# Performance work log

Measured on AMD Instinct MI355X. Metric: run time of the kernel, lower is better.

The kernel has to match this reference:

```python
import jax, jax.numpy as jnp
import numpy as np

N = 50000      # nodes
E = 800000     # edges (last N are self-loops)
F_IN = 128     # n_feats
D = 64         # embedding_size (per-head out dim)
H = 3          # num_heads
G = 1024       # graphs in batch


def setup_inputs() -> dict:
    key = jax.random.key(0)
    ks = jax.random.split(key, 16)
    feats = jax.random.normal(ks[0], (N, F_IN), dtype=jnp.float32)
    # edges: random part + self-loops so every node has in-degree >= 1
    rs = jax.random.randint(ks[1], (E - N,), 0, N)
    rd = jax.random.randint(ks[2], (E - N,), 0, N)
    loops = jnp.arange(N)
    src = jnp.concatenate([rs, loops]).astype(jnp.int32)
    dst = jnp.concatenate([rd, loops]).astype(jnp.int32)
    graph_ids = jnp.sort(jax.random.randint(ks[3], (N,), 0, G)).astype(jnp.int32)

    def nrm(k, shape, fan_in):
        return jax.random.normal(k, shape, dtype=jnp.float32) * (1.0 / np.sqrt(fan_in))

    # gat1A params (DGL GATConv: fc no-bias, attn_l/attn_r [H,D], bias [H*D])
    W1 = nrm(ks[4], (F_IN, H * D), F_IN)
    al1 = nrm(ks[5], (H, D), D)
    ar1 = nrm(ks[6], (H, D), D)
    b1 = jnp.zeros((H * D,), jnp.float32)
    # gatn params (shared across the 2 loop iterations)
    W2 = nrm(ks[7], (D, H * D), D)
    al2 = nrm(ks[8], (H, D), D)
    ar2 = nrm(ks[9], (H, D), D)
    b2 = jnp.zeros((H * D,), jnp.float32)
    # linear1A (shared)
    Wl = nrm(ks[10], (H * D, D), H * D)
    bl = jnp.zeros((D,), jnp.float32)
    return {"feats": feats, "src": src, "dst": dst, "graph_ids": graph_ids,
            "W1": W1, "al1": al1, "ar1": ar1, "b1": b1,
            "W2": W2, "al2": al2, "ar2": ar2, "b2": b2,
            "Wl": Wl, "bl": bl}


def gat_conv(h, W, al, ar, b, src, dst):
    # h: [N, Fin] -> z: [N, H, D]
    z = (h @ W).reshape(-1, H, D)
    el = jnp.sum(z * al, axis=-1)   # [N, H]
    er = jnp.sum(z * ar, axis=-1)   # [N, H]
    e = jax.nn.leaky_relu(el[src] + er[dst], negative_slope=0.2)  # [E, H]
    # edge softmax over incoming edges of each dst node
    m = jax.ops.segment_max(e, dst, num_segments=N)
    ex = jnp.exp(e - m[dst])
    denom = jax.ops.segment_sum(ex, dst, num_segments=N)
    alpha = ex / denom[dst]                              # [E, H]
    msg = z[src] * alpha[:, :, None]                     # [E, H, D]
    out = jax.ops.segment_sum(msg, dst, num_segments=N)  # [N, H, D]
    return out + b.reshape(H, D)


def reference(feats, src, dst, graph_ids, W1, al1, ar1, b1, W2, al2, ar2, b2, Wl, bl):
    x = gat_conv(feats, W1, al1, ar1, b1, src, dst)   # [N, H, D]
    x = x.reshape(N, H * D)
    x = x @ Wl + bl                                   # [N, D]
    for _ in range(2):
        x = gat_conv(x, W2, al2, ar2, b2, src, dst)
        x = x.reshape(N, H * D)
        x = x @ Wl + bl
        # nn.LeakyReLU(True) -> negative_slope = 1.0 -> identity (faithful)
    # AvgPooling: per-graph mean of node features
    sums = jax.ops.segment_sum(x, graph_ids, num_segments=G)           # [G, D]
    cnts = jax.ops.segment_sum(jnp.ones((N,), x.dtype), graph_ids, num_segments=G)
    return sums / jnp.maximum(cnts, 1.0)[:, None]
```

## Files before the change

### kernel.cpp

```cpp
#include <hip/hip_runtime.h>
#include <hip/hip_bf16.h>

#define NN 50000
#define NE 800000
#define FIN 128
#define NHEADS 3
#define NG 1024
#define HD 192

typedef unsigned short ushort_t;
typedef __bf16 bf16x8 __attribute__((ext_vector_type(8)));
typedef float f32x4 __attribute__((ext_vector_type(4)));

__device__ __forceinline__ float bf2f(ushort_t u) {
    union { unsigned int i; float f; } c;
    c.i = ((unsigned int)u) << 16;
    return c.f;
}
__device__ __forceinline__ ushort_t f2bf(float f) {
    __hip_bfloat16 h = __float2bfloat16(f);
    return *reinterpret_cast<ushort_t*>(&h);
}

__global__ __launch_bounds__(256) void fconv_kernel(const float* __restrict__ f,
                                                    ushort_t* __restrict__ fb, int n4) {
    int i = blockIdx.x * 256 + threadIdx.x;
    if (i < n4) {
        float4 v = ((const float4*)f)[i];
        ushort4 o;
        o.x = f2bf(v.x); o.y = f2bf(v.y); o.z = f2bf(v.z); o.w = f2bf(v.w);
        ((ushort4*)fb)[i] = o;
    }
}

__global__ __launch_bounds__(256) void wconv_kernel(const float* __restrict__ W,
                                                    ushort_t* __restrict__ Wt, int K, int N) {
    int idx = blockIdx.x * 256 + threadIdx.x;
    if (idx < K * N) {
        int k = idx / N, n = idx - k * N;
        Wt[n * K + k] = f2bf(W[idx]);
    }
}

template<int K, int NT, int ATTN>
__global__ __launch_bounds__(256) void mgemm_kernel(const ushort_t* __restrict__ Ab,
                                                    const ushort_t* __restrict__ Wt,
                                                    const float* __restrict__ bias,
                                                    const float* __restrict__ al,
                                                    const float* __restrict__ ar,
                                                    float* __restrict__ el4,
                                                    float* __restrict__ er4,
                                                    float* __restrict__ xf,
                                                    ushort_t* __restrict__ xb,
                                                    ushort_t* __restrict__ zb,
                                                    int nrows) {
    constexpr int N = NT * 16;
    const int lane = threadIdx.x & 63;
    const int wid = threadIdx.x >> 6;
    const int row0 = blockIdx.x * 64 + wid * 16;
    const int m = lane & 15;
    const int kg = lane >> 4;

    int rA = row0 + m;
    if (rA > nrows - 1) rA = nrows - 1;
    const ushort_t* arow = Ab + (size_t)rA * K + kg * 8;

    const f32x4 zero4 = {0.f, 0.f, 0.f, 0.f};
    f32x4 acc[NT];
#pragma unroll
    for (int n = 0; n < NT; ++n) acc[n] = zero4;

#pragma unroll
    for (int k0 = 0; k0 < K; k0 += 32) {
        bf16x8 a = *(const bf16x8*)(arow + k0);
#pragma unroll
        for (int n = 0; n < NT; ++n) {
            bf16x8 b = *(const bf16x8*)(Wt + (size_t)(n * 16 + m) * K + k0 + kg * 8);
            acc[n] = __builtin_amdgcn_mfma_f32_16x16x32_bf16(a, b, acc[n], 0, 0, 0);
        }
    }

    const int orow = row0 + kg * 4;

    if (ATTN) {
        float sl[NHEADS][4], sr[NHEADS][4];
#pragma unroll
        for (int h = 0; h < NHEADS; ++h)
#pragma unroll
            for (int r = 0; r < 4; ++r) { sl[h][r] = 0.f; sr[h][r] = 0.f; }
#pragma unroll
        for (int n = 0; n < NT; ++n) {
            float alv = al[n * 16 + m];
            float arv = ar[n * 16 + m];
            const int h = n >> 2;
#pragma unroll
            for (int r = 0; r < 4; ++r) {
                sl[h][r] = fmaf(acc[n][r], alv, sl[h][r]);
                sr[h][r] = fmaf(acc[n][r], arv, sr[h][r]);
            }
        }
#pragma unroll
        for (int off = 1; off < 16; off <<= 1) {
#pragma unroll
            for (int h = 0; h < NHEADS; ++h)
#pragma unroll
                for (int r = 0; r < 4; ++r) {
                    sl[h][r] += __shfl_xor(sl[h][r], off);
                    sr[h][r] += __shfl_xor(sr[h][r], off);
                }
        }
#pragma unroll
        for (int r = 0; r < 4; ++r) {
            int gr = orow + r;
            if (gr < nrows) {
#pragma unroll
                for (int n = 0; n < NT; ++n)
                    zb[(size_t)gr * N + n * 16 + m] = f2bf(acc[n][r]);
                if (m == 0) {
                    *(float4*)(el4 + (size_t)gr * 4) = make_float4(sl[0][r], sl[1][r], sl[2][r], 0.f);
                    *(float4*)(er4 + (size_t)gr * 4) = make_float4(sr[0][r], sr[1][r], sr[2][r], 0.f);
                }
            }
        }
    } else {
#pragma unroll
        for (int r = 0; r < 4; ++r) {
            int gr = orow + r;
            if (gr < nrows) {
#pragma unroll
                for (int n = 0; n < NT; ++n) {
                    float v = acc[n][r] + bias[n * 16 + m];
                    xf[(size_t)gr * N + n * 16 + m] = v;
                    xb[(size_t)gr * N + n * 16 + m] = f2bf(v);
                }
            }
        }
    }
}

__global__ __launch_bounds__(256) void count_kernel(const int* __restrict__ dst,
                                                    int* __restrict__ cnt,
                                                    int* __restrict__ rank) {
    int e0 = blockIdx.x * 1024 + threadIdx.x;
#pragma unroll
    for (int k = 0; k < 4; ++k) {
        int e = e0 + k * 256;
        if (e < NE) rank[e] = atomicAdd(&cnt[dst[e]], 1);
    }
}

__global__ __launch_bounds__(256) void scan_block_kernel(const int* __restrict__ cnt,
                                                         int* __restrict__ incl,
                                                         int* __restrict__ bsum, int n) {
    __shared__ int s[256];
    int tid = threadIdx.x;
    int i = blockIdx.x * 256 + tid;
    int v = (i < n) ? cnt[i] : 0;
    s[tid] = v;
    __syncthreads();
#pragma unroll
    for (int off = 1; off < 256; off <<= 1) {
        int add = (tid >= off) ? s[tid - off] : 0;
        __syncthreads();
        s[tid] += add;
        __syncthreads();
    }
    if (i < n) incl[i] = s[tid];
    if (tid == 255) bsum[blockIdx.x] = s[255];
}

__global__ __launch_bounds__(256) void scan_bsum_kernel(int* __restrict__ bsum, int nb) {
    __shared__ int s[256];
    int tid = threadIdx.x;
    int v = (tid < nb) ? bsum[tid] : 0;
    s[tid] = v;
    __syncthreads();
#pragma unroll
    for (int off = 1; off < 256; off <<= 1) {
        int add = (tid >= off) ? s[tid - off] : 0;
        __syncthreads();
        s[tid] += add;
        __syncthreads();
    }
    if (tid < nb) bsum[tid] = s[tid] - v;
}

__global__ __launch_bounds__(256) void finalize_rowptr_kernel(const int* __restrict__ incl,
                                                              const int* __restrict__ boff,
                                                              int* __restrict__ row_ptr, int n) {
    int i = blockIdx.x * 256 + threadIdx.x;
    if (i < n) row_ptr[i + 1] = incl[i] + boff[i >> 8];
    if (i == 0) row_ptr[0] = 0;
}

__global__ __launch_bounds__(256) void fill_kernel(const int* __restrict__ src,
                                                   const int* __restrict__ dst,
                                                   const int* __restrict__ row_ptr,
                                                   const int* __restrict__ rank,
                                                   int* __restrict__ srcs_sorted) {
    int e = blockIdx.x * 256 + threadIdx.x;
    if (e < NE) {
        srcs_sorted[row_ptr[dst[e]] + rank[e]] = src[e];
    }
}

__global__ __launch_bounds__(256) void aggregate_kernel(const ushort_t* __restrict__ zb,
                                                        const float* __restrict__ el4,
                                                        const float* __restrict__ er4,
                                                        const int* __restrict__ row_ptr,
                                                        const int* __restrict__ srcs,
                                                        const float* __restrict__ bias,
                                                        ushort_t* __restrict__ yb) {
    __shared__ float plds[4][NHEADS][64];
    int node = blockIdx.x * 4 + (threadIdx.x >> 6);
    int lane = threadIdx.x & 63;
    if (node >= NN) return;
    int s0 = row_ptr[node], s1 = row_ptr[node + 1];
    size_t o = (size_t)node * HD;
    const int wid = threadIdx.x >> 6;
    const int h = lane >> 4;
    const int loff = lane * 4;

    float4 erv = *(const float4*)(er4 + (size_t)node * 4);

    float d0 = 0.f, d1 = 0.f, d2 = 0.f;
    f32x4 a = {0.f, 0.f, 0.f, 0.f};

    for (int c0 = s0; c0 < s1; c0 += 64) {
        int i = c0 + lane;
        float p0 = 0.f, p1 = 0.f, p2 = 0.f;
        int s = 0;
        if (i < s1) {
            s = srcs[i];
            float4 elv = *(const float4*)(el4 + (size_t)s * 4);
            float e0 = elv.x + erv.x, e1 = elv.y + erv.y, e2 = elv.z + erv.z;
            e0 = e0 > 0.f ? e0 : 0.2f * e0;
            e1 = e1 > 0.f ? e1 : 0.2f * e1;
            e2 = e2 > 0.f ? e2 : 0.2f * e2;
            p0 = __expf(fminf(e0, 60.f));
            p1 = __expf(fminf(e1, 60.f));
            p2 = __expf(fminf(e2, 60.f));
        }
        d0 += p0; d1 += p1; d2 += p2;
        plds[wid][0][lane] = p0;
        plds[wid][1][lane] = p1;
        plds[wid][2][lane] = p2;
        asm volatile("s_waitcnt lgkmcnt(0)" ::: "memory");
        int nch = s1 - c0; if (nch > 64) nch = 64;
        if (lane < 48) {
            const float* prow = &plds[wid][h][0];
            for (int j = 0; j < nch; j += 4) {
                int sj0 = __builtin_amdgcn_readlane(s, j);
                int sj1 = __builtin_amdgcn_readlane(s, j + 1);
                int sj2 = __builtin_amdgcn_readlane(s, j + 2);
                int sj3 = __builtin_amdgcn_readlane(s, j + 3);
                const ushort_t* r0 = zb + (size_t)sj0 * HD;
                const ushort_t* r1 = zb + (size_t)sj1 * HD;
                const ushort_t* r2 = zb + (size_t)sj2 * HD;
                const ushort_t* r3 = zb + (size_t)sj3 * HD;
                ushort4 zv0 = *(const ushort4*)(r0 + loff);
                ushort4 zv1 = *(const ushort4*)(r1 + loff);
                ushort4 zv2 = *(const ushort4*)(r2 + loff);
                ushort4 zv3 = *(const ushort4*)(r3 + loff);
                float4 q = *(const float4*)(prow + j);
                a[0] = fmaf(q.x, bf2f(zv0.x), a[0]);
                a[1] = fmaf(q.x, bf2f(zv0.y), a[1]);
                a[2] = fmaf(q.x, bf2f(zv0.z), a[2]);
                a[3] = fmaf(q.x, bf2f(zv0.w), a[3]);
                a[0] = fmaf(q.y, bf2f(zv1.x), a[0]);
                a[1] = fmaf(q.y, bf2f(zv1.y), a[1]);
                a[2] = fmaf(q.y, bf2f(zv1.z), a[2]);
                a[3] = fmaf(q.y, bf2f(zv1.w), a[3]);
                a[0] = fmaf(q.z, bf2f(zv2.x), a[0]);
                a[1] = fmaf(q.z, bf2f(zv2.y), a[1]);
                a[2] = fmaf(q.z, bf2f(zv2.z), a[2]);
                a[3] = fmaf(q.z, bf2f(zv2.w), a[3]);
                a[0] = fmaf(q.w, bf2f(zv3.x), a[0]);
                a[1] = fmaf(q.w, bf2f(zv3.y), a[1]);
                a[2] = fmaf(q.w, bf2f(zv3.z), a[2]);
                a[3] = fmaf(q.w, bf2f(zv3.w), a[3]);
            }
        }
    }
#pragma unroll
    for (int off = 32; off > 0; off >>= 1) {
        d0 += __shfl_xor(d0, off);
        d1 += __shfl_xor(d1, off);
        d2 += __shfl_xor(d2, off);
    }

    if (lane < 48) {
        float dd = (h == 0) ? d0 : ((h == 1) ? d1 : d2);
        float rinv = 1.0f / dd;
        float4 bb = *(const float4*)(bias + loff);
        ushort4 ov;
        ov.x = f2bf(a[0] * rinv + bb.x);
        ov.y = f2bf(a[1] * rinv + bb.y);
        ov.z = f2bf(a[2] * rinv + bb.z);
        ov.w = f2bf(a[3] * rinv + bb.w);
        *(ushort4*)(yb + o + loff) = ov;
    }
}

__global__ __launch_bounds__(256) void pool_kernel(const float* __restrict__ x,
                                                   const int* __restrict__ gid,
                                                   float* __restrict__ gsum,
                                                   int* __restrict__ gcnt) {
    int w = blockIdx.x * 4 + (threadIdx.x >> 6);
    int lane = threadIdx.x & 63;
    int n0 = w * 16;
    if (n0 >= NN) return;
    int n1 = n0 + 16; if (n1 > NN) n1 = NN;
    int curg = gid[n0];
    float acc = 0.f;
    int cl = 0;
    for (int n = n0; n < n1; ++n) {
        int g = gid[n];
        if (g != curg) {
            atomicAdd(&gsum[curg * 64 + lane], acc);
            if (lane == 0) atomicAdd(&gcnt[curg], cl);
            acc = 0.f; cl = 0; curg = g;
        }
        acc += x[(size_t)n * 64 + lane];
        cl++;
    }
    atomicAdd(&gsum[curg * 64 + lane], acc);
    if (lane == 0) atomicAdd(&gcnt[curg], cl);
}

__global__ __launch_bounds__(256) void pool_final_kernel(const float* __restrict__ gsum,
                                                         const int* __restrict__ gcnt,
                                                         float* __restrict__ out) {
    int idx = blockIdx.x * 256 + threadIdx.x;
    if (idx < NG * 64) {
        int g = idx >> 6;
        float c = (float)gcnt[g];
        out[idx] = gsum[idx] / fmaxf(c, 1.0f);
    }
}

extern "C" void kernel_launch(void* const* d_in, const int* in_sizes, int n_in,
                              void* d_out, int out_size, void* d_ws, size_t ws_size,
                              hipStream_t stream) {
    const float* feats = (const float*)d_in[0];
    const int* src = (const int*)d_in[1];
    const int* dst = (const int*)d_in[2];
    const int* gid = (const int*)d_in[3];
    const float* W1 = (const float*)d_in[4];
    const float* al1 = (const float*)d_in[5];
    const float* ar1 = (const float*)d_in[6];
    const float* b1 = (const float*)d_in[7];
    const float* W2 = (const float*)d_in[8];
    const float* al2 = (const float*)d_in[9];
    const float* ar2 = (const float*)d_in[10];
    const float* b2 = (const float*)d_in[11];
    const float* Wl = (const float*)d_in[12];
    const float* bl = (const float*)d_in[13];
    float* out = (float*)d_out;

    size_t off = 0;
    auto alloc = [&](size_t bytes) -> char* {
        char* p = (char*)d_ws + off;
        off += (bytes + 255) & ~(size_t)255;
        return p;
    };
    ushort_t* featsb = (ushort_t*)alloc((size_t)NN * FIN * 2);
    ushort_t* zb = (ushort_t*)alloc((size_t)NN * HD * 2);
    ushort_t* yb = (ushort_t*)alloc((size_t)NN * HD * 2);
    ushort_t* xb = (ushort_t*)alloc((size_t)NN * 64 * 2);
    float* xf = (float*)alloc((size_t)NN * 64 * 4);
    float* el4 = (float*)alloc((size_t)NN * 4 * 4);
    float* er4 = (float*)alloc((size_t)NN * 4 * 4);
    ushort_t* W1t = (ushort_t*)alloc((size_t)HD * FIN * 2);
    ushort_t* W2t = (ushort_t*)alloc((size_t)HD * 64 * 2);
    ushort_t* Wlt = (ushort_t*)alloc((size_t)64 * HD * 2);
    int* row_ptr = (int*)alloc((size_t)(NN + 1) * 4);
    int* cnt = (int*)alloc((size_t)NN * 4);
    int* incl = (int*)alloc((size_t)NN * 4);
    int* bsum = (int*)alloc(256 * 4);
    int* rank = (int*)alloc((size_t)NE * 4);
    int* srcs = (int*)alloc((size_t)NE * 4);
    float* gsum = (float*)alloc((size_t)NG * 64 * 4);
    int* gcnt = (int*)alloc((size_t)NG * 4);

    const int nbScan = (NN + 255) / 256;
    const int gridE = (NE + 255) / 256;
    const int gridNode = (NN + 3) / 4;
    const int gridGemm = (NN + 63) / 64;

    fconv_kernel<<<(NN * FIN / 4 + 255) / 256, 256, 0, stream>>>(feats, featsb, NN * FIN / 4);
    wconv_kernel<<<(FIN * HD + 255) / 256, 256, 0, stream>>>(W1, W1t, FIN, HD);
    wconv_kernel<<<(64 * HD + 255) / 256, 256, 0, stream>>>(W2, W2t, 64, HD);
    wconv_kernel<<<(HD * 64 + 255) / 256, 256, 0, stream>>>(Wl, Wlt, HD, 64);

    hipMemsetAsync(cnt, 0, (size_t)NN * 4, stream);
    count_kernel<<<(NE + 1023) / 1024, 256, 0, stream>>>(dst, cnt, rank);
    scan_block_kernel<<<nbScan, 256, 0, stream>>>(cnt, incl, bsum, NN);
    scan_bsum_kernel<<<1, 256, 0, stream>>>(bsum, nbScan);
    finalize_rowptr_kernel<<<nbScan, 256, 0, stream>>>(incl, bsum, row_ptr, NN);
    fill_kernel<<<gridE, 256, 0, stream>>>(src, dst, row_ptr, rank, srcs);

    mgemm_kernel<FIN, 12, 1><<<gridGemm, 256, 0, stream>>>(featsb, W1t, nullptr, al1, ar1,
                                                           el4, er4, nullptr, nullptr, zb, NN);
    aggregate_kernel<<<gridNode, 256, 0, stream>>>(zb, el4, er4, row_ptr, srcs, b1, yb);
    mgemm_kernel<HD, 4, 0><<<gridGemm, 256, 0, stream>>>(yb, Wlt, bl, nullptr, nullptr,
                                                         nullptr, nullptr, xf, xb, nullptr, NN);

    for (int it = 0; it < 2; ++it) {
        mgemm_kernel<64, 12, 1><<<gridGemm, 256, 0, stream>>>(xb, W2t, nullptr, al2, ar2,
                                                              el4, er4, nullptr, nullptr, zb, NN);
        aggregate_kernel<<<gridNode, 256, 0, stream>>>(zb, el4, er4, row_ptr, srcs, b2, yb);
        mgemm_kernel<HD, 4, 0><<<gridGemm, 256, 0, stream>>>(yb, Wlt, bl, nullptr, nullptr,
                                                             nullptr, nullptr, xf, xb, nullptr, NN);
    }

    hipMemsetAsync(gsum, 0, (size_t)NG * 64 * 4 + (size_t)NG * 4, stream);
    pool_kernel<<<(NN / 16 + 3) / 4 + 1, 256, 0, stream>>>(xf, gid, gsum, gcnt);
    pool_final_kernel<<<(NG * 64 + 255) / 256, 256, 0, stream>>>(gsum, gcnt, out);
}
```

Baseline: 436.3 us.

## Merge conversion kernels, fold bsum scan, drop fp32 x, unroll gather by 8

Folds the feature and three weight conversion kernels into one launch, and drops the separate block-sum scan kernel by having each finalize block reduce the preceding block sums with a wave shuffle. It stops writing the fp32 copy of x and has pooling read the bf16 copy, which saves store bandwidth but pools from bf16-rounded values. The aggregation gather is unrolled to 8 neighbour rows per step to keep more loads in flight, and the LDS probability rows are padded. These reduce launch count and memory traffic at a small accuracy cost.

Result: faster. 418.1 us (-4.2%).

```diff
diff --git a/kernel.cpp b/kernel.cpp
--- a/kernel.cpp
+++ b/kernel.cpp
@@ -22,23 +22,42 @@
     return *reinterpret_cast<ushort_t*>(&h);
 }
 
-__global__ __launch_bounds__(256) void fconv_kernel(const float* __restrict__ f,
-                                                    ushort_t* __restrict__ fb, int n4) {
+#define F4 (NN * FIN / 4)
+#define W1E (FIN * HD)
+#define W2E (64 * HD)
+#define WLE (HD * 64)
+__global__ __launch_bounds__(256) void conv_all_kernel(const float* __restrict__ feats,
+                                                       const float* __restrict__ W1,
+                                                       const float* __restrict__ W2,
+                                                       const float* __restrict__ Wl,
+                                                       ushort_t* __restrict__ featsb,
+                                                       ushort_t* __restrict__ W1t,
+                                                       ushort_t* __restrict__ W2t,
+                                                       ushort_t* __restrict__ Wlt) {
     int i = blockIdx.x * 256 + threadIdx.x;
-    if (i < n4) {
-        float4 v = ((const float4*)f)[i];
+    if (i < F4) {
+        float4 v = ((const float4*)feats)[i];
         ushort4 o;
         o.x = f2bf(v.x); o.y = f2bf(v.y); o.z = f2bf(v.z); o.w = f2bf(v.w);
-        ((ushort4*)fb)[i] = o;
-    }
-}
-
-__global__ __launch_bounds__(256) void wconv_kernel(const float* __restrict__ W,
-                                                    ushort_t* __restrict__ Wt, int K, int N) {
-    int idx = blockIdx.x * 256 + threadIdx.x;
-    if (idx < K * N) {
-        int k = idx / N, n = idx - k * N;
-        Wt[n * K + k] = f2bf(W[idx]);
+        ((ushort4*)featsb)[i] = o;
+        return;
+    }
+    int t = i - F4;
+    if (t < W1E) {
+        int k = t / HD, n = t - k * HD;
+        W1t[n * FIN + k] = f2bf(W1[t]);
+        return;
+    }
+    t -= W1E;
+    if (t < W2E) {
+        int k = t / HD, n = t - k * HD;
+        W2t[n * 64 + k] = f2bf(W2[t]);
+        return;
+    }
+    t -= W2E;
+    if (t < WLE) {
+        int k = t / 64, n = t - k * 64;
+        Wlt[n * HD + k] = f2bf(Wl[t]);
     }
 }
 
@@ -50,7 +69,6 @@
                                                     const float* __restrict__ ar,
                                                     float* __restrict__ el4,
                                                     float* __restrict__ er4,
-                                                    float* __restrict__ xf,
                                                     ushort_t* __restrict__ xb,
                                                     ushort_t* __restrict__ zb,
                                                     int nrows) {
@@ -128,11 +146,8 @@
             int gr = orow + r;
             if (gr < nrows) {
 #pragma unroll
-                for (int n = 0; n < NT; ++n) {
-                    float v = acc[n][r] + bias[n * 16 + m];
-                    xf[(size_t)gr * N + n * 16 + m] = v;
-                    xb[(size_t)gr * N + n * 16 + m] = f2bf(v);
-                }
+                for (int n = 0; n < NT; ++n)
+                    xb[(size_t)gr * N + n * 16 + m] = f2bf(acc[n][r] + bias[n * 16 + m]);
             }
         }
     }
@@ -169,27 +184,16 @@
     if (tid == 255) bsum[blockIdx.x] = s[255];
 }
 
-__global__ __launch_bounds__(256) void scan_bsum_kernel(int* __restrict__ bsum, int nb) {
-    __shared__ int s[256];
-    int tid = threadIdx.x;
-    int v = (tid < nb) ? bsum[tid] : 0;
-    s[tid] = v;
-    __syncthreads();
-#pragma unroll
-    for (int off = 1; off < 256; off <<= 1) {
-        int add = (tid >= off) ? s[tid - off] : 0;
-        __syncthreads();
-        s[tid] += add;
-        __syncthreads();
-    }
-    if (tid < nb) bsum[tid] = s[tid] - v;
-}
-
 __global__ __launch_bounds__(256) void finalize_rowptr_kernel(const int* __restrict__ incl,
-                                                              const int* __restrict__ boff,
+                                                              const int* __restrict__ bsum,
                                                               int* __restrict__ row_ptr, int n) {
-    int i = blockIdx.x * 256 + threadIdx.x;
-    if (i < n) row_ptr[i + 1] = incl[i] + boff[i >> 8];
+    int b = blockIdx.x;
+    int part = 0;
+    for (int k = (threadIdx.x & 63); k < b; k += 64) part += bsum[k];
+#pragma unroll
+    for (int off = 32; off > 0; off >>= 1) part += __shfl_xor(part, off);
+    int i = b * 256 + threadIdx.x;
+    if (i < n) row_ptr[i + 1] = incl[i] + part;
     if (i == 0) row_ptr[0] = 0;
 }
 
@@ -211,7 +215,7 @@
                                                         const int* __restrict__ srcs,
                                                         const float* __restrict__ bias,
                                                         ushort_t* __restrict__ yb) {
-    __shared__ float plds[4][NHEADS][64];
+    __shared__ float plds[4][NHEADS][72];
     int node = blockIdx.x * 4 + (threadIdx.x >> 6);
     int lane = threadIdx.x & 63;
     if (node >= NN) return;
@@ -249,36 +253,23 @@
         int nch = s1 - c0; if (nch > 64) nch = 64;
         if (lane < 48) {
             const float* prow = &plds[wid][h][0];
-            for (int j = 0; j < nch; j += 4) {
-                int sj0 = __builtin_amdgcn_readlane(s, j);
-                int sj1 = __builtin_amdgcn_readlane(s, j + 1);
-                int sj2 = __builtin_amdgcn_readlane(s, j + 2);
-                int sj3 = __builtin_amdgcn_readlane(s, j + 3);
-                const ushort_t* r0 = zb + (size_t)sj0 * HD;
-                const ushort_t* r1 = zb + (size_t)sj1 * HD;
-                const ushort_t* r2 = zb + (size_t)sj2 * HD;
-                const ushort_t* r3 = zb + (size_t)sj3 * HD;
-                ushort4 zv0 = *(const ushort4*)(r0 + loff);
-                ushort4 zv1 = *(const ushort4*)(r1 + loff);
-                ushort4 zv2 = *(const ushort4*)(r2 + loff);
-                ushort4 zv3 = *(const ushort4*)(r3 + loff);
-                float4 q = *(const float4*)(prow + j);
-                a[0] = fmaf(q.x, bf2f(zv0.x), a[0]);
-                a[1] = fmaf(q.x, bf2f(zv0.y), a[1]);
-                a[2] = fmaf(q.x, bf2f(zv0.z), a[2]);
-                a[3] = fmaf(q.x, bf2f(zv0.w), a[3]);
-                a[0] = fmaf(q.y, bf2f(zv1.x), a[0]);
-                a[1] = fmaf(q.y, bf2f(zv1.y), a[1]);
-                a[2] = fmaf(q.y, bf2f(zv1.z), a[2]);
-                a[3] = fmaf(q.y, bf2f(zv1.w), a[3]);
-                a[0] = fmaf(q.z, bf2f(zv2.x), a[0]);
-                a[1] = fmaf(q.z, bf2f(zv2.y), a[1]);
-                a[2] = fmaf(q.z, bf2f(zv2.z), a[2]);
-                a[3] = fmaf(q.z, bf2f(zv2.w), a[3]);
-                a[0] = fmaf(q.w, bf2f(zv3.x), a[0]);
-                a[1] = fmaf(q.w, bf2f(zv3.y), a[1]);
-                a[2] = fmaf(q.w, bf2f(zv3.z), a[2]);
-                a[3] = fmaf(q.w, bf2f(zv3.w), a[3]);
+            for (int j = 0; j < nch; j += 8) {
+                ushort4 zv[8];
+#pragma unroll
+                for (int t = 0; t < 8; ++t) {
+                    int sj = __builtin_amdgcn_readlane(s, j + t);
+                    zv[t] = *(const ushort4*)(zb + (size_t)sj * HD + loff);
+                }
+                float4 qa = *(const float4*)(prow + j);
+                float4 qb = *(const float4*)(prow + j + 4);
+                float qq[8] = {qa.x, qa.y, qa.z, qa.w, qb.x, qb.y, qb.z, qb.w};
+#pragma unroll
+                for (int t = 0; t < 8; ++t) {
+                    a[0] = fmaf(qq[t], bf2f(zv[t].x), a[0]);
+                    a[1] = fmaf(qq[t], bf2f(zv[t].y), a[1]);
+                    a[2] = fmaf(qq[t], bf2f(zv[t].z), a[2]);
+                    a[3] = fmaf(qq[t], bf2f(zv[t].w), a[3]);
+                }
             }
         }
     }
@@ -302,7 +293,7 @@
     }
 }
 
-__global__ __launch_bounds__(256) void pool_kernel(const float* __restrict__ x,
+__global__ __launch_bounds__(256) void pool_kernel(const ushort_t* __restrict__ xb,
                                                    const int* __restrict__ gid,
                                                    float* __restrict__ gsum,
                                                    int* __restrict__ gcnt) {
@@ -321,7 +312,7 @@
             if (lane == 0) atomicAdd(&gcnt[curg], cl);
             acc = 0.f; cl = 0; curg = g;
         }
-        acc += x[(size_t)n * 64 + lane];
+        acc += bf2f(xb[(size_t)n * 64 + lane]);
         cl++;
     }
     atomicAdd(&gsum[curg * 64 + lane], acc);
@@ -368,7 +359,6 @@
     ushort_t* zb = (ushort_t*)alloc((size_t)NN * HD * 2);
     ushort_t* yb = (ushort_t*)alloc((size_t)NN * HD * 2);
     ushort_t* xb = (ushort_t*)alloc((size_t)NN * 64 * 2);
-    float* xf = (float*)alloc((size_t)NN * 64 * 4);
     float* el4 = (float*)alloc((size_t)NN * 4 * 4);
     float* er4 = (float*)alloc((size_t)NN * 4 * 4);
     ushort_t* W1t = (ushort_t*)alloc((size_t)HD * FIN * 2);
@@ -388,33 +378,30 @@
     const int gridNode = (NN + 3) / 4;
     const int gridGemm = (NN + 63) / 64;
 
-    fconv_kernel<<<(NN * FIN / 4 + 255) / 256, 256, 0, stream>>>(feats, featsb, NN * FIN / 4);
-    wconv_kernel<<<(FIN * HD + 255) / 256, 256, 0, stream>>>(W1, W1t, FIN, HD);
-    wconv_kernel<<<(64 * HD + 255) / 256, 256, 0, stream>>>(W2, W2t, 64, HD);
-    wconv_kernel<<<(HD * 64 + 255) / 256, 256, 0, stream>>>(Wl, Wlt, HD, 64);
+    conv_all_kernel<<<(F4 + W1E + W2E + WLE + 255) / 256, 256, 0, stream>>>(
+        feats, W1, W2, Wl, featsb, W1t, W2t, Wlt);
 
     hipMemsetAsync(cnt, 0, (size_t)NN * 4, stream);
     count_kernel<<<(NE + 1023) / 1024, 256, 0, stream>>>(dst, cnt, rank);
     scan_block_kernel<<<nbScan, 256, 0, stream>>>(cnt, incl, bsum, NN);
-    scan_bsum_kernel<<<1, 256, 0, stream>>>(bsum, nbScan);
     finalize_rowptr_kernel<<<nbScan, 256, 0, stream>>>(incl, bsum, row_ptr, NN);
     fill_kernel<<<gridE, 256, 0, stream>>>(src, dst, row_ptr, rank, srcs);
 
     mgemm_kernel<FIN, 12, 1><<<gridGemm, 256, 0, stream>>>(featsb, W1t, nullptr, al1, ar1,
-                                                           el4, er4, nullptr, nullptr, zb, NN);
+                                                           el4, er4, nullptr, zb, NN);
     aggregate_kernel<<<gridNode, 256, 0, stream>>>(zb, el4, er4, row_ptr, srcs, b1, yb);
     mgemm_kernel<HD, 4, 0><<<gridGemm, 256, 0, stream>>>(yb, Wlt, bl, nullptr, nullptr,
-                                                         nullptr, nullptr, xf, xb, nullptr, NN);
+                                                         nullptr, nullptr, xb, nullptr, NN);
 
     for (int it = 0; it < 2; ++it) {
         mgemm_kernel<64, 12, 1><<<gridGemm, 256, 0, stream>>>(xb, W2t, nullptr, al2, ar2,
-                                                              el4, er4, nullptr, nullptr, zb, NN);
+                                                              el4, er4, nullptr, zb, NN);
         aggregate_kernel<<<gridNode, 256, 0, stream>>>(zb, el4, er4, row_ptr, srcs, b2, yb);
         mgemm_kernel<HD, 4, 0><<<gridGemm, 256, 0, stream>>>(yb, Wlt, bl, nullptr, nullptr,
-                                                             nullptr, nullptr, xf, xb, nullptr, NN);
+                                                             nullptr, nullptr, xb, nullptr, NN);
     }
 
     hipMemsetAsync(gsum, 0, (size_t)NG * 64 * 4 + (size_t)NG * 4, stream);
-    pool_kernel<<<(NN / 16 + 3) / 4 + 1, 256, 0, stream>>>(xf, gid, gsum, gcnt);
+    pool_kernel<<<(NN / 16 + 3) / 4 + 1, 256, 0, stream>>>(xb, gid, gsum, gcnt);
     pool_final_kernel<<<(NG * 64 + 255) / 256, 256, 0, stream>>>(gsum, gcnt, out);
 }
```
